# Kernel tuning notes

Hardware: AMD Instinct MI355X
Metric: run time of the kernel (lower is better)

## Reference

```python
import jax, jax.numpy as jnp
import numpy as np

BN_EPS = 1e-5


def setup_inputs() -> dict:
    key = jax.random.key(0)
    ks = jax.random.split(key, 6)
    P, D_IN, H, N_NODES = 2_000_000, 3, 128, 20_000
    x = jax.random.normal(ks[0], (P, D_IN), dtype=jnp.float32)
    batch_idx = jax.random.randint(ks[1], (P,), 0, N_NODES, dtype=jnp.int64)
    W1 = jax.random.normal(ks[2], (D_IN, H), dtype=jnp.float32) * 0.5
    b1 = jax.random.normal(ks[3], (H,), dtype=jnp.float32) * 0.1
    gamma = jnp.ones((H,), dtype=jnp.float32)
    beta = jnp.zeros((H,), dtype=jnp.float32)
    running_mean = jnp.zeros((H,), dtype=jnp.float32)
    running_var = jnp.ones((H,), dtype=jnp.float32)
    W2 = jax.random.normal(ks[4], (H, H), dtype=jnp.float32) * (1.0 / np.sqrt(H))
    b2 = jax.random.normal(ks[5], (H,), dtype=jnp.float32) * 0.1
    return {"x": x, "batch_idx": batch_idx, "num_nodes": N_NODES,
            "W1": W1, "b1": b1, "gamma": gamma, "beta": beta,
            "running_mean": running_mean, "running_var": running_var,
            "W2": W2, "b2": b2}


def reference(x, batch_idx, num_nodes, W1, b1, gamma, beta,
              running_mean, running_var, W2, b2):
    # per-point MLP: Linear -> BatchNorm1d (eval: running stats) -> ReLU -> Linear -> ReLU
    h = x @ W1 + b1                                        # [P, H]
    h = (h - running_mean) * jax.lax.rsqrt(running_var + BN_EPS) * gamma + beta
    h = jax.nn.relu(h)
    h = jax.nn.relu(h @ W2 + b2)                            # [P, H], values >= 0
    # scatter_max by node; torch_scatter fills empty segments with 0,
    # and since h >= 0 post-ReLU, clamping the -inf fill to 0 is exact.
    node_feats = jax.ops.segment_max(h, batch_idx, num_segments=num_nodes)
    return jnp.maximum(node_feats, 0.0)                     # [num_nodes, H]
```

## Files before the change

### kernel.cpp

```cpp
#include <hip/hip_runtime.h>
#include <hip/hip_bf16.h>

#define H 128
#define TILE_PTS 32
#define ROW_STRIDE 136
#define NBLK 192
#define BT 1024
#define BSH 4
#define NPB (1 << BSH)
#define CAP 2048
#define RAWN (CAP + 32)
#define HBUF (TILE_PTS * ROW_STRIDE)

typedef __attribute__((ext_vector_type(8))) short short8;
typedef __attribute__((ext_vector_type(4))) float float4v;
typedef __attribute__((ext_vector_type(2))) float float2v;
typedef __attribute__((ext_vector_type(4))) int int4v;

static __device__ __forceinline__ unsigned short f2bf(float f) {
    unsigned u = __float_as_uint(f);
    unsigned r = (u + 0x7fffu + ((u >> 16) & 1u)) >> 16;
    return (unsigned short)r;
}
static __device__ __forceinline__ unsigned pkbf(float a, float b) {
    __hip_bfloat162 h = __float22bfloat162_rn(float2{a, b});
    return *reinterpret_cast<unsigned*>(&h);
}
static __device__ __forceinline__ unsigned short f2h(float f) {
    _Float16 h = (_Float16)f;
    unsigned short u;
    __builtin_memcpy(&u, &h, 2);
    return u;
}
static __device__ __forceinline__ float h2f(unsigned short us) {
    _Float16 h;
    __builtin_memcpy(&h, &us, 2);
    return (float)h;
}

__global__ __launch_bounds__(BT)
void scatter_slot(const int* __restrict__ bidx, const float* __restrict__ x,
                  const float* __restrict__ W2, unsigned short* __restrict__ W2T,
                  int* __restrict__ gcnt, uint2* __restrict__ xb,
                  int P, int nbuk) {
    extern __shared__ int lh[];
    const int b = blockIdx.x, t = threadIdx.x;
    for (int i = b * BT + t; i < H * H; i += NBLK * BT) {
        int n = i >> 7, k = i & 127;
        W2T[i] = f2bf(W2[k * H + n]);
    }
    for (int i = t; i < nbuk; i += BT) lh[i] = 0;
    __syncthreads();
    const int chunk4 = (((P + NBLK - 1) / NBLK) + 3) & ~3;
    const int lo = b * chunk4;
    const int hi = (lo + chunk4 < P) ? lo + chunk4 : P;
    for (int p4 = lo + 4 * t; p4 < hi; p4 += 4 * BT) {
        if (p4 + 4 <= hi) {
            int4v i4 = *(const int4v*)&bidx[p4];
            atomicAdd(&lh[i4.x >> BSH], 1);
            atomicAdd(&lh[i4.y >> BSH], 1);
            atomicAdd(&lh[i4.z >> BSH], 1);
            atomicAdd(&lh[i4.w >> BSH], 1);
        } else {
            for (int p = p4; p < hi; ++p) atomicAdd(&lh[bidx[p] >> BSH], 1);
        }
    }
    __syncthreads();
    for (int i = t; i < nbuk; i += BT) {
        int c = lh[i];
        lh[i] = (c > 0) ? atomicAdd(&gcnt[i], c) : 0;
    }
    __syncthreads();
    auto emit = [&](int idx, float x0, float x1, float x2) {
        int pos = atomicAdd(&lh[idx >> BSH], 1);
        if (pos < CAP) {
            uint2 r;
            r.x = (unsigned)f2h(x0) | ((unsigned)f2h(x1) << 16);
            r.y = (unsigned)f2h(x2) | ((unsigned)(idx & (NPB - 1)) << 16);
            xb[(size_t)(idx >> BSH) * CAP + pos] = r;
        }
    };
    for (int p4 = lo + 4 * t; p4 < hi; p4 += 4 * BT) {
        if (p4 + 4 <= hi) {
            int4v i4 = *(const int4v*)&bidx[p4];
            float4v xa = *(const float4v*)(x + (size_t)p4 * 3);
            float4v xbv = *(const float4v*)(x + (size_t)p4 * 3 + 4);
            float4v xc = *(const float4v*)(x + (size_t)p4 * 3 + 8);
            emit(i4.x, xa[0], xa[1], xa[2]);
            emit(i4.y, xa[3], xbv[0], xbv[1]);
            emit(i4.z, xbv[2], xbv[3], xc[0]);
            emit(i4.w, xc[1], xc[2], xc[3]);
        } else {
            for (int p = p4; p < hi; ++p)
                emit(bidx[p], x[p * 3 + 0], x[p * 3 + 1], x[p * 3 + 2]);
        }
    }
}

__global__ __launch_bounds__(256, 4)
void node_kernel9(const uint2* __restrict__ xb, const int* __restrict__ gcnt,
                  const float* __restrict__ W1, const float* __restrict__ b1,
                  const float* __restrict__ gamma, const float* __restrict__ beta,
                  const float* __restrict__ rmean, const float* __restrict__ rvar,
                  const unsigned short* __restrict__ W2T, const float* __restrict__ b2,
                  float* __restrict__ out, int N)
{
    __shared__ __align__(16) unsigned short pool[2 * HBUF];
    __shared__ __align__(16) uint2 srt[RAWN];
    __shared__ int basec[NPB + 1];
    __shared__ int cur[NPB];

    const int bk   = blockIdx.x;
    const int t    = threadIdx.x;
    const int lane = t & 63;
    const int wave = t >> 6;
    const int g  = t & 15;
    const int q  = t >> 4;
    const int c0 = g * 8;

    float2v w1f2[3][4], b1f2[4];
    #pragma unroll
    for (int jp = 0; jp < 4; ++jp) {
        #pragma unroll
        for (int e = 0; e < 2; ++e) {
            int c = c0 + 2 * jp + e;
            float sc = gamma[c] * rsqrtf(rvar[c] + 1e-5f);
            w1f2[0][jp][e] = W1[0 * H + c] * sc;
            w1f2[1][jp][e] = W1[1 * H + c] * sc;
            w1f2[2][jp][e] = W1[2 * H + c] * sc;
            b1f2[jp][e]    = (b1[c] - rmean[c]) * sc + beta[c];
        }
    }

    const int bn = lane & 15;
    const int kq = (lane >> 4) * 8;
    short8 bfrag[2][4];
    float  b2v[2];
    #pragma unroll
    for (int nt = 0; nt < 2; ++nt) {
        const int nn = wave * 32 + nt * 16 + bn;
        b2v[nt] = b2[nn];
        #pragma unroll
        for (int kk = 0; kk < 4; ++kk)
            bfrag[nt][kk] = *(const short8*)&W2T[nn * H + kk * 32 + kq];
    }

    uint2* raw = (uint2*)pool;
    int n_b = gcnt[bk];
    if (n_b > CAP) n_b = CAP;
    const uint2* src = xb + (size_t)bk * CAP;
    for (int p = t; p < n_b; p += 256) raw[p] = src[p];
    if (t < NPB) cur[t] = 0;
    __syncthreads();
    for (int p = t; p < n_b; p += 256)
        atomicAdd(&cur[raw[p].y >> 16], 1);
    __syncthreads();
    if (t == 0) {
        int run = 0;
        #pragma unroll
        for (int i = 0; i < NPB; ++i) { int c = cur[i]; basec[i] = run; run += c; }
        basec[NPB] = run;
    }
    __syncthreads();
    if (t < NPB) cur[t] = basec[t];
    __syncthreads();
    for (int p = t; p < n_b; p += 256) {
        uint2 r = raw[p];
        int pos = atomicAdd(&cur[r.y >> 16], 1);
        srt[pos] = r;
    }
    for (int p = n_b + t; p < n_b + TILE_PTS; p += 256)
        if (p < RAWN) srt[p] = uint2{0u, 0u};
    __syncthreads();

    const float4v zero4 = {0.f, 0.f, 0.f, 0.f};
    const float NEG_INF = -__builtin_inff();
    const float2v zero2 = {0.f, 0.f};
    const int nodebase = bk << BSH;
    const int nlocal = (N - nodebase < NPB) ? (N - nodebase) : NPB;

    const int st0 = q * ROW_STRIDE + c0;
    const int st1 = (q + 16) * ROW_STRIDE + c0;
    const int ar  = bn * ROW_STRIDE + kq;

    #define STAGE_PT(r, hs, so)                                            \
    {                                                                      \
        float x0 = h2f((unsigned short)((r).x & 0xffffu));                 \
        float x1 = h2f((unsigned short)((r).x >> 16));                     \
        float x2 = h2f((unsigned short)((r).y & 0xffffu));                 \
        float2v a0 = {x0, x0}, a1 = {x1, x1}, a2 = {x2, x2};               \
        int4v pk;                                                          \
        _Pragma("unroll")                                                  \
        for (int jp = 0; jp < 4; ++jp) {                                   \
            float2v hh = b1f2[jp];                                         \
            hh = __builtin_elementwise_fma(a0, w1f2[0][jp], hh);           \
            hh = __builtin_elementwise_fma(a1, w1f2[1][jp], hh);           \
            hh = __builtin_elementwise_fma(a2, w1f2[2][jp], hh);           \
            hh = __builtin_elementwise_max(hh, zero2);                     \
            pk[jp] = (int)pkbf(hh[0], hh[1]);                              \
        }                                                                  \
        *(int4v*)(void*)&(hs)[so] = pk;                                    \
    }

    for (int j = 0; j < nlocal; ++j) {
        const int startj = basec[j];
        const int n      = basec[j + 1] - startj;
        const int ntiles = (n + TILE_PTS - 1) >> 5;

        float2v vm0 = {NEG_INF, NEG_INF};
        float2v vm1 = {NEG_INF, NEG_INF};

        if (ntiles > 0) {
            unsigned short* hb = pool;
            unsigned short* hs = pool + HBUF;
            {
                uint2 r0 = srt[startj + q];
                uint2 r1 = srt[startj + q + 16];
                STAGE_PT(r0, hb, st0);
                STAGE_PT(r1, hb, st1);
            }
            __syncthreads();

            for (int tile = 0; tile < ntiles; ++tile) {
                const int tb = tile * TILE_PTS;
                const bool have = (tile + 1 < ntiles);

                uint2 n0, n1;
                if (have) {
                    n0 = srt[startj + tb + TILE_PTS + q];
                    n1 = srt[startj + tb + TILE_PTS + 16 + q];
                }

                float4v acc00, acc01, acc10, acc11;
                {
                    short8 a0v = *(const short8*)(const void*)&hb[ar];
                    short8 a1v = *(const short8*)(const void*)&hb[ar + 16 * ROW_STRIDE];
                    acc00 = __builtin_amdgcn_mfma_f32_16x16x32_bf16(a0v, bfrag[0][0], zero4, 0, 0, 0);
                    acc01 = __builtin_amdgcn_mfma_f32_16x16x32_bf16(a0v, bfrag[1][0], zero4, 0, 0, 0);
                    acc10 = __builtin_amdgcn_mfma_f32_16x16x32_bf16(a1v, bfrag[0][0], zero4, 0, 0, 0);
                    acc11 = __builtin_amdgcn_mfma_f32_16x16x32_bf16(a1v, bfrag[1][0], zero4, 0, 0, 0);
                }
                #pragma unroll
                for (int kk = 1; kk < 4; ++kk) {
                    short8 a0v = *(const short8*)(const void*)&hb[ar + kk * 32];
                    short8 a1v = *(const short8*)(const void*)&hb[ar + 16 * ROW_STRIDE + kk * 32];
                    acc00 = __builtin_amdgcn_mfma_f32_16x16x32_bf16(a0v, bfrag[0][kk], acc00, 0, 0, 0);
                    acc01 = __builtin_amdgcn_mfma_f32_16x16x32_bf16(a0v, bfrag[1][kk], acc01, 0, 0, 0);
                    acc10 = __builtin_amdgcn_mfma_f32_16x16x32_bf16(a1v, bfrag[0][kk], acc10, 0, 0, 0);
                    acc11 = __builtin_amdgcn_mfma_f32_16x16x32_bf16(a1v, bfrag[1][kk], acc11, 0, 0, 0);
                }

                if (have) {
                    STAGE_PT(n0, hs, st0);
                    STAGE_PT(n1, hs, st1);
                }

                if (tb + TILE_PTS <= n) {
                    vm0 = __builtin_elementwise_max(vm0, float2v{acc00[0], acc00[1]});
                    vm0 = __builtin_elementwise_max(vm0, float2v{acc00[2], acc00[3]});
                    vm0 = __builtin_elementwise_max(vm0, float2v{acc10[0], acc10[1]});
                    vm0 = __builtin_elementwise_max(vm0, float2v{acc10[2], acc10[3]});
                    vm1 = __builtin_elementwise_max(vm1, float2v{acc01[0], acc01[1]});
                    vm1 = __builtin_elementwise_max(vm1, float2v{acc01[2], acc01[3]});
                    vm1 = __builtin_elementwise_max(vm1, float2v{acc11[0], acc11[1]});
                    vm1 = __builtin_elementwise_max(vm1, float2v{acc11[2], acc11[3]});
                } else {
                    const int r0base = (lane >> 4) * 4;
                    #pragma unroll
                    for (int r = 0; r < 4; ++r) {
                        const bool v0 = (tb + r0base + r) < n;
                        const bool v1 = (tb + 16 + r0base + r) < n;
                        vm0[r & 1] = fmaxf(vm0[r & 1], v0 ? acc00[r] : NEG_INF);
                        vm1[r & 1] = fmaxf(vm1[r & 1], v0 ? acc01[r] : NEG_INF);
                        vm0[r & 1] = fmaxf(vm0[r & 1], v1 ? acc10[r] : NEG_INF);
                        vm1[r & 1] = fmaxf(vm1[r & 1], v1 ? acc11[r] : NEG_INF);
                    }
                }
                __syncthreads();
                unsigned short* tmp = hb; hb = hs; hs = tmp;
            }
        }

        float vmax0 = fmaxf(vm0[0], vm0[1]);
        float vmax1 = fmaxf(vm1[0], vm1[1]);
        vmax0 = fmaxf(vmax0, __shfl_xor(vmax0, 16, 64));
        vmax0 = fmaxf(vmax0, __shfl_xor(vmax0, 32, 64));
        vmax1 = fmaxf(vmax1, __shfl_xor(vmax1, 16, 64));
        vmax1 = fmaxf(vmax1, __shfl_xor(vmax1, 32, 64));
        if (lane < 16) {
            float* orow = out + (size_t)(nodebase + j) * H + wave * 32;
            orow[lane]      = fmaxf(vmax0 + b2v[0], 0.f);
            orow[16 + lane] = fmaxf(vmax1 + b2v[1], 0.f);
        }
    }
    #undef STAGE_PT
}

__global__ void histB_kernel(const int* __restrict__ bidx, int* __restrict__ counts, int P) {
    int p = blockIdx.x * 256 + threadIdx.x;
    if (p < P) atomicAdd(&counts[bidx[p]], 1);
}
__global__ __launch_bounds__(1024)
void scanB_kernel(const int* __restrict__ counts, int* __restrict__ starts,
                  int* __restrict__ cursor, int N) {
    __shared__ int sums[1024];
    const int t = threadIdx.x;
    const int chunk = (N + 1023) >> 10;
    const int lo = t * chunk;
    const int hi = (lo + chunk < N) ? lo + chunk : N;
    int s = 0;
    for (int i = lo; i < hi; ++i) s += counts[i];
    sums[t] = s;
    __syncthreads();
    #pragma unroll
    for (int off = 1; off < 1024; off <<= 1) {
        int a = (t >= off) ? sums[t - off] : 0;
        __syncthreads();
        sums[t] += a;
        __syncthreads();
    }
    int run = sums[t] - s;
    for (int i = lo; i < hi; ++i) { starts[i] = run; cursor[i] = run; run += counts[i]; }
    if (t == 1023) starts[N] = sums[1023];
}
__global__ void scatterB_kernel(const int* __restrict__ bidx, const float* __restrict__ x,
                                int* __restrict__ cursor, uint2* __restrict__ xs, int P) {
    int p = blockIdx.x * 256 + threadIdx.x;
    if (p < P) {
        int pos = atomicAdd(&cursor[bidx[p]], 1);
        uint2 r;
        r.x = (unsigned)f2h(x[p * 3 + 0]) | ((unsigned)f2h(x[p * 3 + 1]) << 16);
        r.y = (unsigned)f2h(x[p * 3 + 2]);
        xs[pos] = r;
    }
}
__global__ void convw2_kernel(const float* __restrict__ W2, unsigned short* __restrict__ W2T) {
    int i = blockIdx.x * 256 + threadIdx.x;
    if (i < H * H) {
        int n = i >> 7, k = i & 127;
        W2T[i] = f2bf(W2[k * H + n]);
    }
}

__global__ __launch_bounds__(256, 4)
void node_kernelB(const uint2* __restrict__ xs,
                  const int*   __restrict__ starts,
                  const float* __restrict__ W1, const float* __restrict__ b1,
                  const float* __restrict__ gamma, const float* __restrict__ beta,
                  const float* __restrict__ rmean, const float* __restrict__ rvar,
                  const unsigned short* __restrict__ W2T, const float* __restrict__ b2,
                  float* __restrict__ out, int N)
{
    __shared__ __align__(16) unsigned short h1s[2][TILE_PTS * ROW_STRIDE];
    const int t = threadIdx.x, lane = t & 63, wave = t >> 6;
    const int g = t & 15, q = t >> 4, c0 = g * 8;
    float2v w1f2[3][4], b1f2[4];
    #pragma unroll
    for (int jp = 0; jp < 4; ++jp)
        #pragma unroll
        for (int e = 0; e < 2; ++e) {
            int c = c0 + 2 * jp + e;
            float sc = gamma[c] * rsqrtf(rvar[c] + 1e-5f);
            w1f2[0][jp][e] = W1[0 * H + c] * sc;
            w1f2[1][jp][e] = W1[1 * H + c] * sc;
            w1f2[2][jp][e] = W1[2 * H + c] * sc;
            b1f2[jp][e]    = (b1[c] - rmean[c]) * sc + beta[c];
        }
    const int bn = lane & 15, kq = (lane >> 4) * 8;
    short8 bfrag[2][4]; float b2v[2];
    #pragma unroll
    for (int nt = 0; nt < 2; ++nt) {
        const int nn = wave * 32 + nt * 16 + bn;
        b2v[nt] = b2[nn];
        #pragma unroll
        for (int kk = 0; kk < 4; ++kk)
            bfrag[nt][kk] = *(const short8*)&W2T[nn * H + kk * 32 + kq];
    }
    const float4v zero4 = {0.f, 0.f, 0.f, 0.f};
    const float NEG_INF = -__builtin_inff();
    const float2v zero2 = {0.f, 0.f};
    for (int node = blockIdx.x; node < N; node += gridDim.x) {
        const int start = starts[node];
        const int n = starts[node + 1] - start;
        const int ntiles = (n + TILE_PTS - 1) >> 5;
        float2v vmax2[2];
        vmax2[0] = float2v{NEG_INF, NEG_INF};
        vmax2[1] = float2v{NEG_INF, NEG_INF};
        auto loadx = [&](int tb, float xv[2][3]) {
            #pragma unroll
            for (int i = 0; i < 2; ++i) {
                uint2 r = xs[start + tb + q + 16 * i];
                xv[i][0] = h2f((unsigned short)(r.x & 0xffffu));
                xv[i][1] = h2f((unsigned short)(r.x >> 16));
                xv[i][2] = h2f((unsigned short)(r.y & 0xffffu));
            }
        };
        auto stage = [&](const float xv[2][3], unsigned short* buf) {
            #pragma unroll
            for (int i = 0; i < 2; ++i) {
                const int pl = q + 16 * i;
                float2v a0 = {xv[i][0], xv[i][0]};
                float2v a1 = {xv[i][1], xv[i][1]};
                float2v a2 = {xv[i][2], xv[i][2]};
                int4v pk;
                #pragma unroll
                for (int jp = 0; jp < 4; ++jp) {
                    float2v h = b1f2[jp];
                    h = __builtin_elementwise_fma(a0, w1f2[0][jp], h);
                    h = __builtin_elementwise_fma(a1, w1f2[1][jp], h);
                    h = __builtin_elementwise_fma(a2, w1f2[2][jp], h);
                    h = __builtin_elementwise_max(h, zero2);
                    pk[jp] = (int)pkbf(h[0], h[1]);
                }
                *(int4v*)(void*)&buf[pl * ROW_STRIDE + c0] = pk;
            }
        };
        if (ntiles > 0) {
            float xv[2][3];
            loadx(0, xv);
            stage(xv, h1s[0]);
            __syncthreads();
            int pb = 0;
            for (int tile = 0; tile < ntiles; ++tile) {
                const int tb = tile * TILE_PTS;
                const bool havenext = (tile + 1 < ntiles);
                float nx[2][3];
                if (havenext) loadx(tb + TILE_PTS, nx);
                float4v acc[2][2];
                const unsigned short* hb = h1s[pb];
                {
                    short8 a0 = *(const short8*)&hb[bn * ROW_STRIDE + kq];
                    short8 a1 = *(const short8*)&hb[(16 + bn) * ROW_STRIDE + kq];
                    #pragma unroll
                    for (int nt = 0; nt < 2; ++nt) {
                        acc[0][nt] = __builtin_amdgcn_mfma_f32_16x16x32_bf16(a0, bfrag[nt][0], zero4, 0, 0, 0);
                        acc[1][nt] = __builtin_amdgcn_mfma_f32_16x16x32_bf16(a1, bfrag[nt][0], zero4, 0, 0, 0);
                    }
                }
                #pragma unroll
                for (int kk = 1; kk < 4; ++kk) {
                    short8 a0 = *(const short8*)&hb[bn * ROW_STRIDE + kk * 32 + kq];
                    short8 a1 = *(const short8*)&hb[(16 + bn) * ROW_STRIDE + kk * 32 + kq];
                    #pragma unroll
                    for (int nt = 0; nt < 2; ++nt) {
                        acc[0][nt] = __builtin_amdgcn_mfma_f32_16x16x32_bf16(a0, bfrag[nt][kk], acc[0][nt], 0, 0, 0);
                        acc[1][nt] = __builtin_amdgcn_mfma_f32_16x16x32_bf16(a1, bfrag[nt][kk], acc[1][nt], 0, 0, 0);
                    }
                }
                if (havenext) stage(nx, h1s[pb ^ 1]);
                if (tb + TILE_PTS <= n) {
                    #pragma unroll
                    for (int ps = 0; ps < 2; ++ps)
                        #pragma unroll
                        for (int nt = 0; nt < 2; ++nt) {
                            vmax2[nt] = __builtin_elementwise_max(vmax2[nt],
                                          float2v{acc[ps][nt][0], acc[ps][nt][1]});
                            vmax2[nt] = __builtin_elementwise_max(vmax2[nt],
                                          float2v{acc[ps][nt][2], acc[ps][nt][3]});
                        }
                } else {
                    #pragma unroll
                    for (int ps = 0; ps < 2; ++ps)
                        #pragma unroll
                        for (int r = 0; r < 4; ++r) {
                            const int pl = ps * 16 + (lane >> 4) * 4 + r;
                            const bool valid = (tb + pl) < n;
                            vmax2[0][r & 1] = fmaxf(vmax2[0][r & 1], valid ? acc[ps][0][r] : NEG_INF);
                            vmax2[1][r & 1] = fmaxf(vmax2[1][r & 1], valid ? acc[ps][1][r] : NEG_INF);
                        }
                }
                __syncthreads();
                pb ^= 1;
            }
        }
        float vmax0 = fmaxf(vmax2[0][0], vmax2[0][1]);
        float vmax1 = fmaxf(vmax2[1][0], vmax2[1][1]);
        vmax0 = fmaxf(vmax0, __shfl_xor(vmax0, 16, 64));
        vmax0 = fmaxf(vmax0, __shfl_xor(vmax0, 32, 64));
        vmax1 = fmaxf(vmax1, __shfl_xor(vmax1, 16, 64));
        vmax1 = fmaxf(vmax1, __shfl_xor(vmax1, 32, 64));
        if (lane < 16) {
            float* orow = out + (size_t)node * H + wave * 32;
            orow[lane]      = fmaxf(vmax0 + b2v[0], 0.f);
            orow[16 + lane] = fmaxf(vmax1 + b2v[1], 0.f);
        }
    }
}

extern "C" void kernel_launch(void* const* d_in, const int* in_sizes, int n_in,
                              void* d_out, int out_size, void* d_ws, size_t ws_size,
                              hipStream_t stream) {
    const float* x     = (const float*)d_in[0];
    const int*   bidx  = (const int*)  d_in[1];
    const float* W1    = (const float*)d_in[3];
    const float* b1    = (const float*)d_in[4];
    const float* gamma = (const float*)d_in[5];
    const float* beta  = (const float*)d_in[6];
    const float* rmean = (const float*)d_in[7];
    const float* rvar  = (const float*)d_in[8];
    const float* W2    = (const float*)d_in[9];
    const float* b2    = (const float*)d_in[10];
    float* out = (float*)d_out;

    const int P = in_sizes[1];
    const int N = out_size / H;
    const int nbuk = (N + NPB - 1) >> BSH;

    const size_t szW2T = 32768;
    const size_t szG   = (size_t)4 * ((nbuk + 63) & ~63);
    const size_t szXb  = (size_t)8 * ((size_t)CAP * nbuk + 64);
    const size_t needA = szW2T + szG + szXb + 256;
    const size_t lds1  = (size_t)4 * nbuk;

    char* w = (char*)d_ws;

    if (lds1 <= 60000 && ws_size >= needA) {
        unsigned short* W2T = (unsigned short*)w;
        int* gcnt = (int*)(w + szW2T);
        uint2* xb = (uint2*)(w + szW2T + szG);

        hipMemsetAsync(gcnt, 0, (size_t)nbuk * sizeof(int), stream);
        scatter_slot<<<NBLK, BT, lds1, stream>>>(bidx, x, W2, W2T, gcnt, xb, P, nbuk);
        node_kernel9<<<nbuk, 256, 0, stream>>>(xb, gcnt, W1, b1, gamma, beta,
                                               rmean, rvar, W2T, b2, out, N);
        return;
    }

    const int Npad = (N + 63) & ~63;
    const size_t szStarts = (size_t)4 * (Npad + 64);
    const size_t szCnt    = (size_t)4 * Npad;
    const size_t szRec    = (size_t)8 * (P + 64);
    const size_t needB    = szStarts + szW2T + 2 * szCnt + szRec + 256;
    if (ws_size >= needB) {
        int* starts = (int*)w;
        unsigned short* W2T = (unsigned short*)(w + szStarts);
        int* counts = (int*)(w + szStarts + szW2T);
        int* cursor = (int*)(w + szStarts + szW2T + szCnt);
        uint2* xs   = (uint2*)(w + szStarts + szW2T + 2 * szCnt);

        hipMemsetAsync(counts, 0, (size_t)N * sizeof(int), stream);
        const int pblocks = (P + 255) / 256;
        const int grid = (N < 2048) ? N : 2048;
        convw2_kernel<<<(H * H + 255) / 256, 256, 0, stream>>>(W2, W2T);
        histB_kernel<<<pblocks, 256, 0, stream>>>(bidx, counts, P);
        scanB_kernel<<<1, 1024, 0, stream>>>(counts, starts, cursor, N);
        scatterB_kernel<<<pblocks, 256, 0, stream>>>(bidx, x, cursor, xs, P);
        node_kernelB<<<grid, 256, 0, stream>>>(xs, starts, W1, b1, gamma, beta,
                                               rmean, rvar, W2T, b2, out, N);
    }
}
```

Before: 230.8 us.

## Halve node buckets, process two buckets per block, use per-wave sort counters

Buckets now hold 8 nodes instead of 16, with slot capacity halved to match, and the scatter kernel launches 512 blocks instead of 192. Each node-kernel block now handles two consecutive buckets in a loop, so the W1/BN folding and W2 MFMA fragments are loaded once and reused across both. The in-LDS counting sort uses per-wave histogram counters to spread atomic contention. The aim is more parallelism in the scatter stage, cheaper per-bucket setup and a smaller sort working set. The cost is an extra barrier per bucket and a higher chance of a bucket overflowing its smaller capacity.

```diff
diff --git a/kernel.cpp b/kernel.cpp
--- a/kernel.cpp
+++ b/kernel.cpp
@@ -4,11 +4,11 @@
 #define H 128
 #define TILE_PTS 32
 #define ROW_STRIDE 136
-#define NBLK 192
+#define NBLK 512
 #define BT 1024
-#define BSH 4
+#define BSH 3
 #define NPB (1 << BSH)
-#define CAP 2048
+#define CAP 1024
 #define RAWN (CAP + 32)
 #define HBUF (TILE_PTS * ROW_STRIDE)
 
@@ -98,19 +98,18 @@
 }
 
 __global__ __launch_bounds__(256, 4)
-void node_kernel9(const uint2* __restrict__ xb, const int* __restrict__ gcnt,
-                  const float* __restrict__ W1, const float* __restrict__ b1,
-                  const float* __restrict__ gamma, const float* __restrict__ beta,
-                  const float* __restrict__ rmean, const float* __restrict__ rvar,
-                  const unsigned short* __restrict__ W2T, const float* __restrict__ b2,
-                  float* __restrict__ out, int N)
+void node_kernel12(const uint2* __restrict__ xb, const int* __restrict__ gcnt,
+                   const float* __restrict__ W1, const float* __restrict__ b1,
+                   const float* __restrict__ gamma, const float* __restrict__ beta,
+                   const float* __restrict__ rmean, const float* __restrict__ rvar,
+                   const unsigned short* __restrict__ W2T, const float* __restrict__ b2,
+                   float* __restrict__ out, int N, int nbuk)
 {
     __shared__ __align__(16) unsigned short pool[2 * HBUF];
     __shared__ __align__(16) uint2 srt[RAWN];
     __shared__ int basec[NPB + 1];
-    __shared__ int cur[NPB];
-
-    const int bk   = blockIdx.x;
+    __shared__ int curw[4][NPB];
+
     const int t    = threadIdx.x;
     const int lane = t & 63;
     const int wave = t >> 6;
@@ -145,39 +144,9 @@
             bfrag[nt][kk] = *(const short8*)&W2T[nn * H + kk * 32 + kq];
     }
 
-    uint2* raw = (uint2*)pool;
-    int n_b = gcnt[bk];
-    if (n_b > CAP) n_b = CAP;
-    const uint2* src = xb + (size_t)bk * CAP;
-    for (int p = t; p < n_b; p += 256) raw[p] = src[p];
-    if (t < NPB) cur[t] = 0;
-    __syncthreads();
-    for (int p = t; p < n_b; p += 256)
-        atomicAdd(&cur[raw[p].y >> 16], 1);
-    __syncthreads();
-    if (t == 0) {
-        int run = 0;
-        #pragma unroll
-        for (int i = 0; i < NPB; ++i) { int c = cur[i]; basec[i] = run; run += c; }
-        basec[NPB] = run;
-    }
-    __syncthreads();
-    if (t < NPB) cur[t] = basec[t];
-    __syncthreads();
-    for (int p = t; p < n_b; p += 256) {
-        uint2 r = raw[p];
-        int pos = atomicAdd(&cur[r.y >> 16], 1);
-        srt[pos] = r;
-    }
-    for (int p = n_b + t; p < n_b + TILE_PTS; p += 256)
-        if (p < RAWN) srt[p] = uint2{0u, 0u};
-    __syncthreads();
-
     const float4v zero4 = {0.f, 0.f, 0.f, 0.f};
     const float NEG_INF = -__builtin_inff();
     const float2v zero2 = {0.f, 0.f};
-    const int nodebase = bk << BSH;
-    const int nlocal = (N - nodebase < NPB) ? (N - nodebase) : NPB;
 
     const int st0 = q * ROW_STRIDE + c0;
     const int st1 = (q + 16) * ROW_STRIDE + c0;
@@ -202,95 +171,137 @@
         *(int4v*)(void*)&(hs)[so] = pk;                                    \
     }
 
-    for (int j = 0; j < nlocal; ++j) {
-        const int startj = basec[j];
-        const int n      = basec[j + 1] - startj;
-        const int ntiles = (n + TILE_PTS - 1) >> 5;
-
-        float2v vm0 = {NEG_INF, NEG_INF};
-        float2v vm1 = {NEG_INF, NEG_INF};
-
-        if (ntiles > 0) {
-            unsigned short* hb = pool;
-            unsigned short* hs = pool + HBUF;
-            {
-                uint2 r0 = srt[startj + q];
-                uint2 r1 = srt[startj + q + 16];
-                STAGE_PT(r0, hb, st0);
-                STAGE_PT(r1, hb, st1);
+    for (int hf = 0; hf < 2; ++hf) {
+        const int bk = blockIdx.x * 2 + hf;
+        if (bk >= nbuk) break;
+
+        __syncthreads();
+
+        uint2* raw = (uint2*)pool;
+        int n_b = gcnt[bk];
+        if (n_b > CAP) n_b = CAP;
+        const uint2* src = xb + (size_t)bk * CAP;
+        for (int p = t; p < n_b; p += 256) raw[p] = src[p];
+        if (t < 4 * NPB) ((int*)curw)[t] = 0;
+        __syncthreads();
+        for (int p = t; p < n_b; p += 256)
+            atomicAdd(&curw[wave][raw[p].y >> 16], 1);
+        __syncthreads();
+        if (t == 0) {
+            int run = 0;
+            #pragma unroll
+            for (int i = 0; i < NPB; ++i) {
+                basec[i] = run;
+                #pragma unroll
+                for (int w = 0; w < 4; ++w) {
+                    int c = curw[w][i]; curw[w][i] = run; run += c;
+                }
             }
-            __syncthreads();
-
-            for (int tile = 0; tile < ntiles; ++tile) {
-                const int tb = tile * TILE_PTS;
-                const bool have = (tile + 1 < ntiles);
-
-                uint2 n0, n1;
-                if (have) {
-                    n0 = srt[startj + tb + TILE_PTS + q];
-                    n1 = srt[startj + tb + TILE_PTS + 16 + q];
-                }
-
-                float4v acc00, acc01, acc10, acc11;
+            basec[NPB] = run;
+        }
+        __syncthreads();
+        for (int p = t; p < n_b; p += 256) {
+            uint2 r = raw[p];
+            int pos = atomicAdd(&curw[wave][r.y >> 16], 1);
+            srt[pos] = r;
+        }
+        for (int p = n_b + t; p < n_b + TILE_PTS; p += 256)
+            if (p < RAWN) srt[p] = uint2{0u, 0u};
+        __syncthreads();
+
+        const int nodebase = bk << BSH;
+        const int nlocal = (N - nodebase < NPB) ? (N - nodebase) : NPB;
+
+        for (int j = 0; j < nlocal; ++j) {
+            const int startj = basec[j];
+            const int n      = basec[j + 1] - startj;
+            const int ntiles = (n + TILE_PTS - 1) >> 5;
+
+            float2v vm0 = {NEG_INF, NEG_INF};
+            float2v vm1 = {NEG_INF, NEG_INF};
+
+            if (ntiles > 0) {
+                unsigned short* hb = pool;
+                unsigned short* hs = pool + HBUF;
                 {
-                    short8 a0v = *(const short8*)(const void*)&hb[ar];
-                    short8 a1v = *(const short8*)(const void*)&hb[ar + 16 * ROW_STRIDE];
-                    acc00 = __builtin_amdgcn_mfma_f32_16x16x32_bf16(a0v, bfrag[0][0], zero4, 0, 0, 0);
-                    acc01 = __builtin_amdgcn_mfma_f32_16x16x32_bf16(a0v, bfrag[1][0], zero4, 0, 0, 0);
-                    acc10 = __builtin_amdgcn_mfma_f32_16x16x32_bf16(a1v, bfrag[0][0], zero4, 0, 0, 0);
-                    acc11 = __builtin_amdgcn_mfma_f32_16x16x32_bf16(a1v, bfrag[1][0], zero4, 0, 0, 0);
-                }
-                #pragma unroll
-                for (int kk = 1; kk < 4; ++kk) {
-                    short8 a0v = *(const short8*)(const void*)&hb[ar + kk * 32];
-                    short8 a1v = *(const short8*)(const void*)&hb[ar + 16 * ROW_STRIDE + kk * 32];
-                    acc00 = __builtin_amdgcn_mfma_f32_16x16x32_bf16(a0v, bfrag[0][kk], acc00, 0, 0, 0);
-                    acc01 = __builtin_amdgcn_mfma_f32_16x16x32_bf16(a0v, bfrag[1][kk], acc01, 0, 0, 0);
-                    acc10 = __builtin_amdgcn_mfma_f32_16x16x32_bf16(a1v, bfrag[0][kk], acc10, 0, 0, 0);
-                    acc11 = __builtin_amdgcn_mfma_f32_16x16x32_bf16(a1v, bfrag[1][kk], acc11, 0, 0, 0);
-                }
-
-                if (have) {
-                    STAGE_PT(n0, hs, st0);
-                    STAGE_PT(n1, hs, st1);
-                }
-
-                if (tb + TILE_PTS <= n) {
-                    vm0 = __builtin_elementwise_max(vm0, float2v{acc00[0], acc00[1]});
-                    vm0 = __builtin_elementwise_max(vm0, float2v{acc00[2], acc00[3]});
-                    vm0 = __builtin_elementwise_max(vm0, float2v{acc10[0], acc10[1]});
-                    vm0 = __builtin_elementwise_max(vm0, float2v{acc10[2], acc10[3]});
-                    vm1 = __builtin_elementwise_max(vm1, float2v{acc01[0], acc01[1]});
-                    vm1 = __builtin_elementwise_max(vm1, float2v{acc01[2], acc01[3]});
-                    vm1 = __builtin_elementwise_max(vm1, float2v{acc11[0], acc11[1]});
-                    vm1 = __builtin_elementwise_max(vm1, float2v{acc11[2], acc11[3]});
-                } else {
-                    const int r0base = (lane >> 4) * 4;
+                    uint2 r0 = srt[startj + q];
+                    uint2 r1 = srt[startj + q + 16];
+                    STAGE_PT(r0, hb, st0);
+                    STAGE_PT(r1, hb, st1);
+                }
+                __syncthreads();
+
+                for (int tile = 0; tile < ntiles; ++tile) {
+                    const int tb = tile * TILE_PTS;
+                    const bool have = (tile + 1 < ntiles);
+
+                    uint2 n0, n1;
+                    if (have) {
+                        n0 = srt[startj + tb + TILE_PTS + q];
+                        n1 = srt[startj + tb + TILE_PTS + 16 + q];
+                    }
+
+                    float4v acc00, acc01, acc10, acc11;
+                    {
+                        short8 a0v = *(const short8*)(const void*)&hb[ar];
+                        short8 a1v = *(const short8*)(const void*)&hb[ar + 16 * ROW_STRIDE];
+                        acc00 = __builtin_amdgcn_mfma_f32_16x16x32_bf16(a0v, bfrag[0][0], zero4, 0, 0, 0);
+                        acc01 = __builtin_amdgcn_mfma_f32_16x16x32_bf16(a0v, bfrag[1][0], zero4, 0, 0, 0);
+                        acc10 = __builtin_amdgcn_mfma_f32_16x16x32_bf16(a1v, bfrag[0][0], zero4, 0, 0, 0);
+                        acc11 = __builtin_amdgcn_mfma_f32_16x16x32_bf16(a1v, bfrag[1][0], zero4, 0, 0, 0);
+                    }
                     #pragma unroll
-                    for (int r = 0; r < 4; ++r) {
-                        const bool v0 = (tb + r0base + r) < n;
-                        const bool v1 = (tb + 16 + r0base + r) < n;
-                        vm0[r & 1] = fmaxf(vm0[r & 1], v0 ? acc00[r] : NEG_INF);
-                        vm1[r & 1] = fmaxf(vm1[r & 1], v0 ? acc01[r] : NEG_INF);
-                        vm0[r & 1] = fmaxf(vm0[r & 1], v1 ? acc10[r] : NEG_INF);
-                        vm1[r & 1] = fmaxf(vm1[r & 1], v1 ? acc11[r] : NEG_INF);
-                    }
-                }
-                __syncthreads();
-                unsigned short* tmp = hb; hb = hs; hs = tmp;
+                    for (int kk = 1; kk < 4; ++kk) {
+                        short8 a0v = *(const short8*)(const void*)&hb[ar + kk * 32];
+                        short8 a1v = *(const short8*)(const void*)&hb[ar + 16 * ROW_STRIDE + kk * 32];
+                        acc00 = __builtin_amdgcn_mfma_f32_16x16x32_bf16(a0v, bfrag[0][kk], acc00, 0, 0, 0);
+                        acc01 = __builtin_amdgcn_mfma_f32_16x16x32_bf16(a0v, bfrag[1][kk], acc01, 0, 0, 0);
+                        acc10 = __builtin_amdgcn_mfma_f32_16x16x32_bf16(a1v, bfrag[0][kk], acc10, 0, 0, 0);
+                        acc11 = __builtin_amdgcn_mfma_f32_16x16x32_bf16(a1v, bfrag[1][kk], acc11, 0, 0, 0);
+                    }
+
+                    if (have) {
+                        STAGE_PT(n0, hs, st0);
+                        STAGE_PT(n1, hs, st1);
+                    }
+
+                    if (tb + TILE_PTS <= n) {
+                        vm0 = __builtin_elementwise_max(vm0, float2v{acc00[0], acc00[1]});
+                        vm0 = __builtin_elementwise_max(vm0, float2v{acc00[2], acc00[3]});
+                        vm0 = __builtin_elementwise_max(vm0, float2v{acc10[0], acc10[1]});
+                        vm0 = __builtin_elementwise_max(vm0, float2v{acc10[2], acc10[3]});
+                        vm1 = __builtin_elementwise_max(vm1, float2v{acc01[0], acc01[1]});
+                        vm1 = __builtin_elementwise_max(vm1, float2v{acc01[2], acc01[3]});
+                        vm1 = __builtin_elementwise_max(vm1, float2v{acc11[0], acc11[1]});
+                        vm1 = __builtin_elementwise_max(vm1, float2v{acc11[2], acc11[3]});
+                    } else {
+                        const int r0base = (lane >> 4) * 4;
+                        #pragma unroll
+                        for (int r = 0; r < 4; ++r) {
+                            const bool v0 = (tb + r0base + r) < n;
+                            const bool v1 = (tb + 16 + r0base + r) < n;
+                            vm0[r & 1] = fmaxf(vm0[r & 1], v0 ? acc00[r] : NEG_INF);
+                            vm1[r & 1] = fmaxf(vm1[r & 1], v0 ? acc01[r] : NEG_INF);
+                            vm0[r & 1] = fmaxf(vm0[r & 1], v1 ? acc10[r] : NEG_INF);
+                            vm1[r & 1] = fmaxf(vm1[r & 1], v1 ? acc11[r] : NEG_INF);
+                        }
+                    }
+                    __syncthreads();
+                    unsigned short* tmp = hb; hb = hs; hs = tmp;
+                }
             }
-        }
-
-        float vmax0 = fmaxf(vm0[0], vm0[1]);
-        float vmax1 = fmaxf(vm1[0], vm1[1]);
-        vmax0 = fmaxf(vmax0, __shfl_xor(vmax0, 16, 64));
-        vmax0 = fmaxf(vmax0, __shfl_xor(vmax0, 32, 64));
-        vmax1 = fmaxf(vmax1, __shfl_xor(vmax1, 16, 64));
-        vmax1 = fmaxf(vmax1, __shfl_xor(vmax1, 32, 64));
-        if (lane < 16) {
-            float* orow = out + (size_t)(nodebase + j) * H + wave * 32;
-            orow[lane]      = fmaxf(vmax0 + b2v[0], 0.f);
-            orow[16 + lane] = fmaxf(vmax1 + b2v[1], 0.f);
+
+            float vmax0 = fmaxf(vm0[0], vm0[1]);
+            float vmax1 = fmaxf(vm1[0], vm1[1]);
+            vmax0 = fmaxf(vmax0, __shfl_xor(vmax0, 16, 64));
+            vmax0 = fmaxf(vmax0, __shfl_xor(vmax0, 32, 64));
+            vmax1 = fmaxf(vmax1, __shfl_xor(vmax1, 16, 64));
+            vmax1 = fmaxf(vmax1, __shfl_xor(vmax1, 32, 64));
+            if (lane < 16) {
+                float* orow = out + (size_t)(nodebase + j) * H + wave * 32;
+                orow[lane]      = fmaxf(vmax0 + b2v[0], 0.f);
+                orow[16 + lane] = fmaxf(vmax1 + b2v[1], 0.f);
+            }
         }
     }
     #undef STAGE_PT
@@ -521,8 +532,9 @@
 
         hipMemsetAsync(gcnt, 0, (size_t)nbuk * sizeof(int), stream);
         scatter_slot<<<NBLK, BT, lds1, stream>>>(bidx, x, W2, W2T, gcnt, xb, P, nbuk);
-        node_kernel9<<<nbuk, 256, 0, stream>>>(xb, gcnt, W1, b1, gamma, beta,
-                                               rmean, rvar, W2T, b2, out, N);
+        const int nbk2 = (nbuk + 1) >> 1;
+        node_kernel12<<<nbk2, 256, 0, stream>>>(xb, gcnt, W1, b1, gamma, beta,
+                                                rmean, rvar, W2T, b2, out, N, nbuk);
         return;
     }
 
```

After: 245.2 us. +6.2%, slower.
